# Performance work log

Measured on AMD Instinct MI355X. Metric: run time of the kernel, lower is better.

The kernel has to match this reference:

```python
import jax, jax.numpy as jnp
import numpy as np
from jax import lax

BN_EPS = 1e-5


def conv3x3(x, w):
    # x: [B,C,H,W], w: [O,I,3,3] -> [B,O,H,W], stride 1, SAME padding, no bias
    return lax.conv_general_dilated(x, w, (1, 1), 'SAME',
                                    dimension_numbers=('NCHW', 'OIHW', 'NCHW'))


def batchnorm_eval(x, gamma, beta, mean, var):
    inv = gamma / jnp.sqrt(var + BN_EPS)
    return x * inv[None, :, None, None] + (beta - mean * inv)[None, :, None, None]


def avg_pool3(x):
    # AvgPool2d(3, stride=1, padding=1) with count_include_pad=True -> sum/9
    s = lax.reduce_window(x, 0.0, lax.add, (1, 1, 3, 3), (1, 1, 1, 1), 'SAME')
    return s / 9.0


def max_pool3(x):
    return lax.reduce_window(x, -jnp.inf, lax.max, (1, 1, 3, 3), (1, 1, 1, 1), 'SAME')


def setup_inputs() -> dict:
    key = jax.random.key(0)
    ks = jax.random.split(key, 20)
    B, C, H, W = 8, 256, 48, 48
    sc = 0.05
    inp = {
        'ftr': jax.random.normal(ks[0], (B, C, H, W), jnp.float32),
        'wq': jax.random.normal(ks[1], (C, C, 1, 1), jnp.float32) * sc,
        'bq': jax.random.normal(ks[2], (C,), jnp.float32) * sc,
        'wk': jax.random.normal(ks[3], (C, C, 1, 1), jnp.float32) * sc,
        'bk': jax.random.normal(ks[4], (C,), jnp.float32) * sc,
        'wv': jax.random.normal(ks[5], (C, C, 1, 1), jnp.float32) * sc,
        'bv': jax.random.normal(ks[6], (C,), jnp.float32) * sc,
        'delta': jnp.array([0.1], jnp.float32),
        'w_rbc': jax.random.normal(ks[7], (C, C, 3, 3), jnp.float32) * sc,
        'g1': jnp.ones((C,), jnp.float32),
        'b1': jnp.zeros((C,), jnp.float32),
        'm1': jnp.zeros((C,), jnp.float32),
        'v1': jnp.ones((C,), jnp.float32),
        'w_rbc2': jax.random.normal(ks[8], (C, 2 * C, 3, 3), jnp.float32) * sc,
        'g2': jnp.ones((C,), jnp.float32),
        'b2': jnp.zeros((C,), jnp.float32),
        'm2': jnp.zeros((C,), jnp.float32),
        'v2': jnp.ones((C,), jnp.float32),
    }
    return inp


def reference(ftr, wq, bq, wk, bk, wv, bv, delta, w_rbc, g1, b1, m1, v1,
              w_rbc2, g2, b2, m2, v2):
    B, C, H, W = ftr.shape
    P = H * W
    x = ftr.reshape(B, C, P)  # [B,C,P]
    # 1x1 convs as channel matmuls
    q = jnp.einsum('oc,bcp->bop', wq[:, :, 0, 0], x) + bq[None, :, None]
    k = jnp.einsum('oc,bcp->bop', wk[:, :, 0, 0], x) + bk[None, :, None]
    v = jnp.einsum('oc,bcp->bop', wv[:, :, 0, 0], x) + bv[None, :, None]
    # scores[b,i,j] = sum_c q[b,c,i] * k[b,c,j]; softmax over i (dim=1)
    scores = jnp.einsum('bci,bcj->bij', q, k)
    weights = jax.nn.softmax(scores, axis=1)
    G = jnp.einsum('bci,bij->bcj', v, weights).reshape(B, C, H, W)
    out = delta[0] * G + ftr
    # conv_rbc: conv3x3 -> BN(eval) -> ReLU, then sigmoid gate
    out = jax.nn.relu(batchnorm_eval(conv3x3(out, w_rbc), g1, b1, m1, v1))
    gate = jax.nn.sigmoid(out)
    ftr_avg = avg_pool3(ftr) * gate
    ftr_max = max_pool3(ftr) * gate
    cat = jnp.concatenate((ftr_max, ftr_avg), axis=1)  # [B,2C,H,W]
    out = jax.nn.relu(batchnorm_eval(conv3x3(cat, w_rbc2), g2, b2, m2, v2))
    return out
```

## Files before the change

### kernel.cpp

```cpp
#include <hip/hip_runtime.h>
#include <math.h>

#define NB   8
#define CCH  256
#define PPX  2304
#define CPb  (CCH*PPX)
#define NTOT (NB*CPb)
#define PSQ  (PPX*PPX)
#define PADIMG 2500

typedef short short8_t __attribute__((ext_vector_type(8)));
typedef float f4_t __attribute__((ext_vector_type(4)));

__device__ __forceinline__ float relu_(float x){ return x > 0.f ? x : 0.f; }

__device__ __forceinline__ unsigned short f2bf(float f) {
  unsigned int u = __builtin_bit_cast(unsigned int, f);
  u += 0x7fffu + ((u >> 16) & 1u);
  return (unsigned short)(u >> 16);
}
__device__ __forceinline__ float bf2f(unsigned short h) {
  unsigned int u = ((unsigned int)h) << 16;
  return __builtin_bit_cast(float, u);
}
__device__ __forceinline__ unsigned int pack2(float a, float b) {
  return (unsigned int)f2bf(a) | ((unsigned int)f2bf(b) << 16);
}

__device__ __forceinline__ void gll16(const void* g, void* l) {
  __builtin_amdgcn_global_load_lds(
      (const __attribute__((address_space(1))) unsigned int*)g,
      (__attribute__((address_space(3))) unsigned int*)l, 16, 0, 0);
}

__global__ __launch_bounds__(256) void castw(
    const float* __restrict__ w, unsigned short* __restrict__ o, int n)
{
  const int i = blockIdx.x * 256 + threadIdx.x;
  if (i < n) o[i] = f2bf(w[i]);
}

__global__ __launch_bounds__(256) void repack_w(
    const float* __restrict__ w, unsigned short* __restrict__ wr, int Cin)
{
  const int idx = blockIdx.x * 256 + threadIdx.x;
  const int total = 9 * 256 * Cin;
  if (idx >= total) return;
  const int c = idx % Cin;
  const int rest = idx / Cin;
  const int o = rest % 256;
  const int tap = rest / 256;
  wr[idx] = f2bf(w[((size_t)o * Cin + c) * 9 + tap]);
}

__global__ __launch_bounds__(256) void transpose_cast(
    const float* __restrict__ ftr, unsigned short* __restrict__ xt)
{
  const int p0 = blockIdx.x * 64, c0 = blockIdx.y * 64, b = blockIdx.z;
  const int t = threadIdx.x;
  __shared__ unsigned short T[64][72];
  #pragma unroll
  for (int pass = 0; pass < 4; pass++) {
    const int cr = pass * 16 + (t >> 4);
    const int pc = (t & 15) * 4;
    float4 v = *(const float4*)&ftr[((size_t)(b * 256 + c0 + cr)) * PPX + p0 + pc];
    T[pc + 0][cr] = f2bf(v.x); T[pc + 1][cr] = f2bf(v.y);
    T[pc + 2][cr] = f2bf(v.z); T[pc + 3][cr] = f2bf(v.w);
  }
  __syncthreads();
  #pragma unroll
  for (int pass = 0; pass < 2; pass++) {
    const int pr = pass * 32 + (t >> 3);
    const int cc = (t & 7) * 8;
    *(uint4*)&xt[((size_t)(b * PPX + p0 + pr)) * 256 + c0 + cc] = *(const uint4*)&T[pr][cc];
  }
}

template<int EPI>
__global__ __launch_bounds__(256) void gemm_nt(
    const unsigned short* __restrict__ A, long Ab,
    const unsigned short* __restrict__ B, long Bb, int K,
    unsigned short* __restrict__ O, long Ob, int ldo,
    const float* __restrict__ bias,
    const float* __restrict__ ftr, const float* __restrict__ delta, int bstart)
{
  const int t = threadIdx.x;
  const int ln = t & 63;
  const int wid = t >> 6;
  const int wm = (wid & 1) * 64, wn = (wid >> 1) * 64;
  const int lm = ln & 15, lg = ln >> 4;
  const int m0 = blockIdx.x * 128, n0 = blockIdx.y * 128;
  const long bz = blockIdx.z;
  const unsigned short* Ap = A + bz * Ab;
  const unsigned short* Bp = B + bz * Bb;

  __shared__ __align__(16) unsigned short As[128 * 32];
  __shared__ __align__(16) unsigned short Bs[128 * 32];

  const int sR = ln >> 2, sP = ln & 3;
  const int fbase = lm * 32 + (((lg + (lm >> 2)) & 3) * 8);

  f4_t acc[4][4];
  #pragma unroll
  for (int i = 0; i < 4; i++)
    #pragma unroll
    for (int j = 0; j < 4; j++) acc[i][j] = (f4_t){0.f, 0.f, 0.f, 0.f};

  for (int k0 = 0; k0 < K; k0 += 32) {
    __syncthreads();
    #pragma unroll
    for (int i = wid; i < 8; i += 4) {
      const int R = i * 16 + sR;
      const int l = (sP - (R >> 2)) & 3;
      gll16(Ap + (size_t)(m0 + R) * K + k0 + l * 8, As + i * 512);
      gll16(Bp + (size_t)(n0 + R) * K + k0 + l * 8, Bs + i * 512);
    }
    __syncthreads();
    short8_t a[4], b[4];
    #pragma unroll
    for (int ti = 0; ti < 4; ti++)
      a[ti] = *(const short8_t*)(As + (wm + ti * 16) * 32 + fbase);
    #pragma unroll
    for (int tj = 0; tj < 4; tj++)
      b[tj] = *(const short8_t*)(Bs + (wn + tj * 16) * 32 + fbase);
    #pragma unroll
    for (int ti = 0; ti < 4; ti++)
      #pragma unroll
      for (int tj = 0; tj < 4; tj++)
        acc[ti][tj] = __builtin_amdgcn_mfma_f32_16x16x32_bf16(
            a[ti], b[tj], acc[ti][tj], 0, 0, 0);
  }

  if (EPI == 3) {
    const int b = bstart + (int)bz;
    const float d0 = delta[0];
    #pragma unroll
    for (int ti = 0; ti < 4; ti++) {
      const int mb = m0 + wm + ti * 16 + (lg << 2);
      #pragma unroll
      for (int tj = 0; tj < 4; tj++) {
        const int n = n0 + wn + tj * 16 + lm;
        const int y = n / 48, x = n - (n / 48) * 48;
        const size_t pp = (size_t)(y + 1) * 50 + (x + 1);
        float vr[4];
        #pragma unroll
        for (int r = 0; r < 4; r++)
          vr[r] = d0 * acc[ti][tj][r] + ftr[((size_t)(b * 256 + mb + r)) * PPX + n];
        uint2 o;
        o.x = pack2(vr[0], vr[1]);
        o.y = pack2(vr[2], vr[3]);
        *(uint2*)(O + ((size_t)b * PADIMG + pp) * 256 + mb) = o;
      }
    }
  } else {
    #pragma unroll
    for (int ti = 0; ti < 4; ti++) {
      const int mb = m0 + wm + ti * 16 + (lg << 2);
      #pragma unroll
      for (int tj = 0; tj < 4; tj++) {
        const int n = n0 + wn + tj * 16 + lm;
        float add0 = 0.f, add1 = 0.f, add2 = 0.f, add3 = 0.f;
        if (EPI == 1) { add0 = bias[mb]; add1 = bias[mb+1]; add2 = bias[mb+2]; add3 = bias[mb+3]; }
        if (EPI == 2) { add0 = add1 = add2 = add3 = bias[n]; }
        uint2 o;
        o.x = pack2(acc[ti][tj][0] + add0, acc[ti][tj][1] + add1);
        o.y = pack2(acc[ti][tj][2] + add2, acc[ti][tj][3] + add3);
        *(uint2*)(O + bz * Ob + (size_t)n * ldo + mb) = o;
      }
    }
  }
}

template<int EPI>
__global__ __launch_bounds__(256) void gemm64(
    const unsigned short* __restrict__ A, long Ab,
    const unsigned short* __restrict__ B, long Bb, int K,
    unsigned short* __restrict__ O, long Ob, int ldo,
    const float* __restrict__ bias,
    const float* __restrict__ ftr, const float* __restrict__ delta, int bstart)
{
  const int t = threadIdx.x;
  const int ln = t & 63;
  const int wid = t >> 6;
  const int wn = wid * 32;
  const int lm = ln & 15, lg = ln >> 4;
  const int m0 = blockIdx.x * 64, n0 = blockIdx.y * 128;
  const long bz = blockIdx.z;
  const unsigned short* Ap = A + bz * Ab;
  const unsigned short* Bp = B + bz * Bb;

  __shared__ __align__(16) unsigned short As[64 * 32];
  __shared__ __align__(16) unsigned short Bs[128 * 32];

  const int sR = ln >> 2, sP = ln & 3;
  const int fbase = lm * 32 + (((lg + (lm >> 2)) & 3) * 8);

  f4_t acc[4][2];
  #pragma unroll
  for (int i = 0; i < 4; i++)
    #pragma unroll
    for (int j = 0; j < 2; j++) acc[i][j] = (f4_t){0.f, 0.f, 0.f, 0.f};

  for (int k0 = 0; k0 < K; k0 += 32) {
    __syncthreads();
    {
      const int R = wid * 16 + sR;
      const int l = (sP - (R >> 2)) & 3;
      gll16(Ap + (size_t)(m0 + R) * K + k0 + l * 8, As + wid * 512);
    }
    #pragma unroll
    for (int i = wid; i < 8; i += 4) {
      const int R = i * 16 + sR;
      const int l = (sP - (R >> 2)) & 3;
      gll16(Bp + (size_t)(n0 + R) * K + k0 + l * 8, Bs + i * 512);
    }
    __syncthreads();
    short8_t a[4], b[2];
    #pragma unroll
    for (int ti = 0; ti < 4; ti++)
      a[ti] = *(const short8_t*)(As + (ti * 16) * 32 + fbase);
    #pragma unroll
    for (int tj = 0; tj < 2; tj++)
      b[tj] = *(const short8_t*)(Bs + (wn + tj * 16) * 32 + fbase);
    #pragma unroll
    for (int ti = 0; ti < 4; ti++)
      #pragma unroll
      for (int tj = 0; tj < 2; tj++)
        acc[ti][tj] = __builtin_amdgcn_mfma_f32_16x16x32_bf16(
            a[ti], b[tj], acc[ti][tj], 0, 0, 0);
  }

  if (EPI == 3) {
    const int b = bstart + (int)bz;
    const float d0 = delta[0];
    #pragma unroll
    for (int ti = 0; ti < 4; ti++) {
      const int mb = m0 + ti * 16 + (lg << 2);
      #pragma unroll
      for (int tj = 0; tj < 2; tj++) {
        const int n = n0 + wn + tj * 16 + lm;
        const int y = n / 48, x = n - (n / 48) * 48;
        const size_t pp = (size_t)(y + 1) * 50 + (x + 1);
        float vr[4];
        #pragma unroll
        for (int r = 0; r < 4; r++)
          vr[r] = d0 * acc[ti][tj][r] + ftr[((size_t)(b * 256 + mb + r)) * PPX + n];
        uint2 o;
        o.x = pack2(vr[0], vr[1]);
        o.y = pack2(vr[2], vr[3]);
        *(uint2*)(O + ((size_t)b * PADIMG + pp) * 256 + mb) = o;
      }
    }
  } else {
    #pragma unroll
    for (int ti = 0; ti < 4; ti++) {
      const int mb = m0 + ti * 16 + (lg << 2);
      #pragma unroll
      for (int tj = 0; tj < 2; tj++) {
        const int n = n0 + wn + tj * 16 + lm;
        float add0 = 0.f, add1 = 0.f, add2 = 0.f, add3 = 0.f;
        if (EPI == 1) { add0 = bias[mb]; add1 = bias[mb+1]; add2 = bias[mb+2]; add3 = bias[mb+3]; }
        if (EPI == 2) { add0 = add1 = add2 = add3 = bias[n]; }
        uint2 o;
        o.x = pack2(acc[ti][tj][0] + add0, acc[ti][tj][1] + add1);
        o.y = pack2(acc[ti][tj][2] + add2, acc[ti][tj][3] + add3);
        *(uint2*)(O + bz * Ob + (size_t)n * ldo + mb) = o;
      }
    }
  }
}

__global__ __launch_bounds__(256) void rowstats(
    unsigned short* __restrict__ St, long sstride)
{
  const int j = blockIdx.x, bb = blockIdx.y;
  unsigned short* row = St + (long)bb * sstride + (size_t)j * PPX;
  const int t = threadIdx.x;

  float v[16];
  int nv = 0;
  float m = -1e30f;
  for (int ch = t; ch < 288; ch += 256) {
    const uint4 d = *(const uint4*)(row + ch * 8);
    const unsigned int* dp = (const unsigned int*)&d;
    #pragma unroll
    for (int q = 0; q < 4; q++) {
      v[nv]     = bf2f((unsigned short)(dp[q] & 0xffffu));
      v[nv + 1] = bf2f((unsigned short)(dp[q] >> 16));
      m = fmaxf(m, fmaxf(v[nv], v[nv + 1]));
      nv += 2;
    }
  }
  #pragma unroll
  for (int off = 32; off > 0; off >>= 1)
    m = fmaxf(m, __shfl_xor(m, off));
  __shared__ float red[8];
  if ((t & 63) == 0) red[t >> 6] = m;
  __syncthreads();
  m = fmaxf(fmaxf(red[0], red[1]), fmaxf(red[2], red[3]));

  float sum = 0.f;
  for (int u = 0; u < nv; u++) { v[u] = __expf(v[u] - m); sum += v[u]; }
  #pragma unroll
  for (int off = 32; off > 0; off >>= 1)
    sum += __shfl_xor(sum, off);
  if ((t & 63) == 0) red[4 + (t >> 6)] = sum;
  __syncthreads();
  const float inv = 1.f / (red[4] + red[5] + red[6] + red[7]);

  int u = 0;
  for (int ch = t; ch < 288; ch += 256) {
    unsigned int res[4];
    #pragma unroll
    for (int q = 0; q < 4; q++) {
      res[q] = pack2(v[u] * inv, v[u + 1] * inv);
      u += 2;
    }
    *(uint4*)(row + ch * 8) = *(const uint4*)res;
  }
}

template<bool OUT_BF16>
__global__ __launch_bounds__(256) void conv_mfma(
    const unsigned short* __restrict__ act_p, int Cin,
    const unsigned short* __restrict__ wr,
    const float* __restrict__ gamma, const float* __restrict__ beta,
    const float* __restrict__ mean,  const float* __restrict__ var,
    void* __restrict__ outv)
{
  const int t  = threadIdx.x;
  const int wv = t >> 6;
  const int ln = t & 63;
  const int lm = ln & 15;
  const int lg = ln >> 4;

  const int bx = blockIdx.x;
  const int bb = bx / 9;
  const int p0 = (bx % 9) * 256;
  const int m0 = blockIdx.y * 32;

  __shared__ __align__(16) unsigned short As[9 * 32 * 32];
  __shared__ __align__(16) unsigned short Bs[368 * 32];

  const int qbase = p0 + 2 * (p0 / 48);
  int qoff[4];
  #pragma unroll
  for (int tj = 0; tj < 4; tj++) {
    const int p = p0 + wv * 64 + tj * 16 + lm;
    qoff[tj] = (p - p0) + 2 * (p / 48 - p0 / 48) + 51;
  }

  const int sR = ln >> 2, sP = ln & 3;
  const int sl = (sP - (sR >> 2)) & 3;
  const int abase = lm * 32 + (((lg + (lm >> 2)) & 3) * 8);

  const unsigned short* gb = act_p + (size_t)bb * PADIMG * Cin;
  const unsigned short* gsrc = gb + (size_t)(qbase + sR) * Cin + sl * 8;

  f4_t acc[2][4];
  #pragma unroll
  for (int i = 0; i < 2; i++)
    #pragma unroll
    for (int j = 0; j < 4; j++) acc[i][j] = (f4_t){0.f, 0.f, 0.f, 0.f};

  for (int c0 = 0; c0 < Cin; c0 += 32) {
    __syncthreads();
    for (int i = wv; i < 18; i += 4) {
      const int R = i * 16 + sR;
      const int tap = R >> 5, mr = R & 31;
      const int l = (sP - (R >> 2)) & 3;
      gll16(wr + ((size_t)(tap * 256 + m0 + mr)) * Cin + c0 + l * 8, As + i * 512);
    }
    const unsigned short* src = gsrc + c0;
    for (int i = wv; i < 23; i += 4)
      gll16(src + (size_t)i * 16 * Cin, Bs + i * 512);
    __syncthreads();
    #pragma unroll
    for (int ky = 0; ky < 3; ky++) {
      #pragma unroll
      for (int kx = 0; kx < 3; kx++) {
        const int off = (ky - 1) * 50 + (kx - 1);
        const int tap = ky * 3 + kx;
        short8_t a[2], b[4];
        #pragma unroll
        for (int ti = 0; ti < 2; ti++)
          a[ti] = *(const short8_t*)(As + tap * 1024 + ti * 512 + abase);
        #pragma unroll
        for (int tj = 0; tj < 4; tj++) {
          const int R = qoff[tj] + off;
          const int slot = (lg + (R >> 2)) & 3;
          b[tj] = *(const short8_t*)(Bs + R * 32 + slot * 8);
        }
        #pragma unroll
        for (int ti = 0; ti < 2; ti++)
          #pragma unroll
          for (int tj = 0; tj < 4; tj++)
            acc[ti][tj] = __builtin_amdgcn_mfma_f32_16x16x32_bf16(
                a[ti], b[tj], acc[ti][tj], 0, 0, 0);
      }
    }
  }

  #pragma unroll
  for (int ti = 0; ti < 2; ti++) {
    const int m = m0 + ti * 16 + (lg << 2);
    float inv[4], add[4];
    #pragma unroll
    for (int r = 0; r < 4; r++) {
      inv[r] = gamma[m + r] * rsqrtf(var[m + r] + 1e-5f);
      add[r] = beta[m + r] - mean[m + r] * inv[r];
    }
    #pragma unroll
    for (int tj = 0; tj < 4; tj++) {
      const int p = p0 + wv * 64 + tj * 16 + lm;
      float vr[4];
      #pragma unroll
      for (int r = 0; r < 4; r++)
        vr[r] = relu_(acc[ti][tj][r] * inv[r] + add[r]);
      if (OUT_BF16) {
        uint2 o;
        o.x = pack2(vr[0], vr[1]);
        o.y = pack2(vr[2], vr[3]);
        *(uint2*)((unsigned short*)outv + ((size_t)(bb * PPX + p)) * 256 + m) = o;
      } else {
        #pragma unroll
        for (int r = 0; r < 4; r++)
          ((float*)outv)[((size_t)(bb * 256 + m + r)) * PPX + p] = vr[r];
      }
    }
  }
}

__global__ __launch_bounds__(256) void pool_gate_cat(
    const unsigned short* __restrict__ xt, const unsigned short* __restrict__ act1b,
    unsigned short* __restrict__ cat_p)
{
  const int idx = blockIdx.x * 256 + threadIdx.x;
  const int c = idx & 255;
  const int rest = idx >> 8;
  const int p = rest % PPX;
  const int b = rest / PPX;
  const int y = p / 48, x = p - (p / 48) * 48;
  const unsigned short* base = xt + ((size_t)b * PPX) * 256 + c;
  float s = 0.f, mxv = -1e30f;
  #pragma unroll
  for (int dy = -1; dy <= 1; dy++) {
    const int yy = y + dy;
    if (yy < 0 || yy >= 48) continue;
    #pragma unroll
    for (int dx = -1; dx <= 1; dx++) {
      const int xx = x + dx;
      if (xx < 0 || xx >= 48) continue;
      const float f = bf2f(base[(size_t)(yy * 48 + xx) * 256]);
      s += f; mxv = fmaxf(mxv, f);
    }
  }
  const float g = bf2f(act1b[(size_t)idx]);
  const float gate = 1.f / (1.f + __expf(-g));
  const size_t pp = (size_t)(y + 1) * 50 + (x + 1);
  unsigned short* crow = cat_p + ((size_t)b * PADIMG + pp) * 512;
  crow[c]       = f2bf(mxv * gate);
  crow[c + 256] = f2bf(s * (1.f / 9.f) * gate);
}

extern "C" void kernel_launch(void* const* d_in, const int* in_sizes, int n_in,
                              void* d_out, int out_size, void* d_ws, size_t ws_size,
                              hipStream_t stream)
{
  const float* ftr  = (const float*)d_in[0];
  const float* wq   = (const float*)d_in[1];
  const float* bq   = (const float*)d_in[2];
  const float* wk   = (const float*)d_in[3];
  const float* bk   = (const float*)d_in[4];
  const float* wv   = (const float*)d_in[5];
  const float* bv   = (const float*)d_in[6];
  const float* delta= (const float*)d_in[7];
  const float* w1   = (const float*)d_in[8];
  const float* g1   = (const float*)d_in[9];
  const float* b1   = (const float*)d_in[10];
  const float* m1   = (const float*)d_in[11];
  const float* v1   = (const float*)d_in[12];
  const float* w2   = (const float*)d_in[13];
  const float* g2   = (const float*)d_in[14];
  const float* b2   = (const float*)d_in[15];
  const float* m2   = (const float*)d_in[16];
  const float* v2   = (const float*)d_in[17];
  float* out = (float*)d_out;

  const size_t XT = (size_t)NTOT;
  unsigned short* base = (unsigned short*)d_ws;
  unsigned short* xt   = base;
  unsigned short* qt   = xt  + XT;
  unsigned short* kt   = qt  + XT;
  unsigned short* vbuf = kt  + XT;
  unsigned short* wqb  = vbuf + XT;
  unsigned short* wkb  = wqb + 65536;
  unsigned short* wvb  = wkb + 65536;
  unsigned short* wr1  = wvb + 65536;
  unsigned short* wr2  = wr1 + (size_t)9 * 256 * 256;
  unsigned short* attn_p = wr2 + (size_t)9 * 256 * 512;
  unsigned short* act1b  = attn_p + (size_t)NB * PADIMG * 256;
  unsigned short* cat_p  = act1b + XT;
  unsigned short* St     = cat_p + (size_t)NB * PADIMG * 512;

  const size_t head_bytes = (size_t)((char*)St - (char*)base);
  const bool modeA = ws_size >= head_bytes + (size_t)NB * PSQ * 2;

  const size_t ATTN_P_SH = (size_t)NB * PADIMG * 256;
  const size_t CAT_P_SH  = (size_t)NB * PADIMG * 512;

  castw<<<dim3(256), 256, 0, stream>>>(wq, wqb, 65536);
  castw<<<dim3(256), 256, 0, stream>>>(wk, wkb, 65536);
  castw<<<dim3(256), 256, 0, stream>>>(wv, wvb, 65536);
  repack_w<<<dim3((9 * 256 * 256 + 255) / 256), 256, 0, stream>>>(w1, wr1, 256);
  repack_w<<<dim3((9 * 256 * 512 + 255) / 256), 256, 0, stream>>>(w2, wr2, 512);

  transpose_cast<<<dim3(36, 4, 8), 256, 0, stream>>>(ftr, xt);

  gemm64<1><<<dim3(4, 18, 8), 256, 0, stream>>>(
      wqb, 0L, xt, (long)CPb, 256, qt, (long)CPb, 256, bq, nullptr, nullptr, 0);
  gemm64<1><<<dim3(4, 18, 8), 256, 0, stream>>>(
      wkb, 0L, xt, (long)CPb, 256, kt, (long)CPb, 256, bk, nullptr, nullptr, 0);
  gemm64<2><<<dim3(36, 2, 8), 256, 0, stream>>>(
      xt, (long)CPb, wvb, 0L, 256, vbuf, (long)CPb, PPX, bv, nullptr, nullptr, 0);

  hipMemsetAsync(attn_p, 0, ATTN_P_SH * 2, stream);

  if (modeA) {
    gemm_nt<0><<<dim3(18, 18, 8), 256, 0, stream>>>(
        qt, (long)CPb, kt, (long)CPb, 256, St, (long)PSQ, PPX, nullptr, nullptr, nullptr, 0);
    rowstats<<<dim3(PPX, 8), 256, 0, stream>>>(St, (long)PSQ);
    gemm64<3><<<dim3(4, 18, 8), 256, 0, stream>>>(
        vbuf, (long)CPb, St, (long)PSQ, PPX, attn_p, 0L, 0, nullptr, ftr, delta, 0);
  } else {
    for (int b = 0; b < NB; b++) {
      gemm_nt<0><<<dim3(18, 18, 1), 256, 0, stream>>>(
          qt + (size_t)b * CPb, 0L, kt + (size_t)b * CPb, 0L, 256,
          St, 0L, PPX, nullptr, nullptr, nullptr, 0);
      rowstats<<<dim3(PPX, 1), 256, 0, stream>>>(St, 0L);
      gemm64<3><<<dim3(4, 18, 1), 256, 0, stream>>>(
          vbuf + (size_t)b * CPb, 0L, St, 0L, PPX, attn_p, 0L, 0, nullptr, ftr, delta, b);
    }
  }

  conv_mfma<true><<<dim3(72, 8), 256, 0, stream>>>(
      attn_p, 256, wr1, g1, b1, m1, v1, (void*)act1b);

  hipMemsetAsync(cat_p, 0, CAT_P_SH * 2, stream);
  pool_gate_cat<<<dim3(NTOT / 256), 256, 0, stream>>>(xt, act1b, cat_p);

  conv_mfma<false><<<dim3(72, 8), 256, 0, stream>>>(
      cat_p, 512, wr2, g2, b2, m2, v2, (void*)out);
}
```

Before: 434.4 us.

## Fuse softmax exp and normalization into PV GEMM, rowstats writes only max/sum

The rowstats kernel now writes only the per-row max and inverse sum, not the full normalized score matrix. A new 128x128-tile PV GEMM recomputes exp(s - max) on the fly while loading score tiles and applies the 1/sum scaling in the epilogue together with the delta-residual add. This drops one full read-modify-write pass over the large B×P×P score matrix. In exchange the GEMM does extra exp work per element, and each P tile is re-exponentiated for both channel blocks. The stats buffer reuses the wq weight buffer, which is no longer needed at that point.

```diff
diff --git a/kernel.cpp b/kernel.cpp
--- a/kernel.cpp
+++ b/kernel.cpp
@@ -131,28 +131,7 @@
             a[ti], b[tj], acc[ti][tj], 0, 0, 0);
   }
 
-  if (EPI == 3) {
-    const int b = bstart + (int)bz;
-    const float d0 = delta[0];
-    #pragma unroll
-    for (int ti = 0; ti < 4; ti++) {
-      const int mb = m0 + wm + ti * 16 + (lg << 2);
-      #pragma unroll
-      for (int tj = 0; tj < 4; tj++) {
-        const int n = n0 + wn + tj * 16 + lm;
-        const int y = n / 48, x = n - (n / 48) * 48;
-        const size_t pp = (size_t)(y + 1) * 50 + (x + 1);
-        float vr[4];
-        #pragma unroll
-        for (int r = 0; r < 4; r++)
-          vr[r] = d0 * acc[ti][tj][r] + ftr[((size_t)(b * 256 + mb + r)) * PPX + n];
-        uint2 o;
-        o.x = pack2(vr[0], vr[1]);
-        o.y = pack2(vr[2], vr[3]);
-        *(uint2*)(O + ((size_t)b * PADIMG + pp) * 256 + mb) = o;
-      }
-    }
-  } else {
+  {
     #pragma unroll
     for (int ti = 0; ti < 4; ti++) {
       const int mb = m0 + wm + ti * 16 + (lg << 2);
@@ -171,6 +150,100 @@
   }
 }
 
+__global__ __launch_bounds__(256) void gemm_pv(
+    const unsigned short* __restrict__ A, long Ab,
+    const unsigned short* __restrict__ B, long Bb,
+    int K,
+    unsigned short* __restrict__ O,
+    const float* __restrict__ stats,
+    const float* __restrict__ ftr, const float* __restrict__ delta, int bstart)
+{
+  const int t = threadIdx.x;
+  const int ln = t & 63;
+  const int wid = t >> 6;
+  const int wm = (wid & 1) * 64, wn = (wid >> 1) * 64;
+  const int lm = ln & 15, lg = ln >> 4;
+  const int m0 = blockIdx.x * 128, n0 = blockIdx.y * 128;
+  const long bz = blockIdx.z;
+  const int b = bstart + (int)bz;
+  const unsigned short* Ap = A + bz * Ab;
+  const unsigned short* Bp = B + bz * Bb;
+
+  __shared__ __align__(16) unsigned short As[128 * 32];
+  __shared__ __align__(16) unsigned short Bs[128 * 32];
+
+  const int sR = ln >> 2, sP = ln & 3;
+  const int fbase = lm * 32 + (((lg + (lm >> 2)) & 3) * 8);
+
+  float mj[4], ivj[4];
+  #pragma unroll
+  for (int tj = 0; tj < 4; tj++) {
+    const int n = n0 + wn + tj * 16 + lm;
+    const float2 s2 = *(const float2*)&stats[((size_t)b * PPX + n) * 2];
+    mj[tj] = s2.x; ivj[tj] = s2.y;
+  }
+
+  f4_t acc[4][4];
+  #pragma unroll
+  for (int i = 0; i < 4; i++)
+    #pragma unroll
+    for (int j = 0; j < 4; j++) acc[i][j] = (f4_t){0.f, 0.f, 0.f, 0.f};
+
+  for (int k0 = 0; k0 < K; k0 += 32) {
+    __syncthreads();
+    #pragma unroll
+    for (int i = wid; i < 8; i += 4) {
+      const int R = i * 16 + sR;
+      const int l = (sP - (R >> 2)) & 3;
+      gll16(Ap + (size_t)(m0 + R) * K + k0 + l * 8, As + i * 512);
+      gll16(Bp + (size_t)(n0 + R) * K + k0 + l * 8, Bs + i * 512);
+    }
+    __syncthreads();
+    short8_t a[4], b8[4];
+    #pragma unroll
+    for (int ti = 0; ti < 4; ti++)
+      a[ti] = *(const short8_t*)(As + (wm + ti * 16) * 32 + fbase);
+    #pragma unroll
+    for (int tj = 0; tj < 4; tj++) {
+      short8_t raw = *(const short8_t*)(Bs + (wn + tj * 16) * 32 + fbase);
+      short8_t w;
+      #pragma unroll
+      for (int e = 0; e < 8; e++) {
+        const float f = bf2f((unsigned short)raw[e]);
+        w[e] = (short)f2bf(__expf(f - mj[tj]));
+      }
+      b8[tj] = w;
+    }
+    #pragma unroll
+    for (int ti = 0; ti < 4; ti++)
+      #pragma unroll
+      for (int tj = 0; tj < 4; tj++)
+        acc[ti][tj] = __builtin_amdgcn_mfma_f32_16x16x32_bf16(
+            a[ti], b8[tj], acc[ti][tj], 0, 0, 0);
+  }
+
+  const float d0 = delta[0];
+  #pragma unroll
+  for (int ti = 0; ti < 4; ti++) {
+    const int mb = m0 + wm + ti * 16 + (lg << 2);
+    #pragma unroll
+    for (int tj = 0; tj < 4; tj++) {
+      const int n = n0 + wn + tj * 16 + lm;
+      const int y = n / 48, x = n - (n / 48) * 48;
+      const size_t pp = (size_t)(y + 1) * 50 + (x + 1);
+      const float sc = d0 * ivj[tj];
+      float vr[4];
+      #pragma unroll
+      for (int r = 0; r < 4; r++)
+        vr[r] = sc * acc[ti][tj][r] + ftr[((size_t)(b * 256 + mb + r)) * PPX + n];
+      uint2 o;
+      o.x = pack2(vr[0], vr[1]);
+      o.y = pack2(vr[2], vr[3]);
+      *(uint2*)(O + ((size_t)b * PADIMG + pp) * 256 + mb) = o;
+    }
+  }
+}
+
 template<int EPI>
 __global__ __launch_bounds__(256) void gemm64(
     const unsigned short* __restrict__ A, long Ab,
@@ -230,28 +303,7 @@
             a[ti], b[tj], acc[ti][tj], 0, 0, 0);
   }
 
-  if (EPI == 3) {
-    const int b = bstart + (int)bz;
-    const float d0 = delta[0];
-    #pragma unroll
-    for (int ti = 0; ti < 4; ti++) {
-      const int mb = m0 + ti * 16 + (lg << 2);
-      #pragma unroll
-      for (int tj = 0; tj < 2; tj++) {
-        const int n = n0 + wn + tj * 16 + lm;
-        const int y = n / 48, x = n - (n / 48) * 48;
-        const size_t pp = (size_t)(y + 1) * 50 + (x + 1);
-        float vr[4];
-        #pragma unroll
-        for (int r = 0; r < 4; r++)
-          vr[r] = d0 * acc[ti][tj][r] + ftr[((size_t)(b * 256 + mb + r)) * PPX + n];
-        uint2 o;
-        o.x = pack2(vr[0], vr[1]);
-        o.y = pack2(vr[2], vr[3]);
-        *(uint2*)(O + ((size_t)b * PADIMG + pp) * 256 + mb) = o;
-      }
-    }
-  } else {
+  {
     #pragma unroll
     for (int ti = 0; ti < 4; ti++) {
       const int mb = m0 + ti * 16 + (lg << 2);
@@ -271,10 +323,11 @@
 }
 
 __global__ __launch_bounds__(256) void rowstats(
-    unsigned short* __restrict__ St, long sstride)
+    const unsigned short* __restrict__ St, long sstride,
+    float* __restrict__ stats, int bstart)
 {
   const int j = blockIdx.x, bb = blockIdx.y;
-  unsigned short* row = St + (long)bb * sstride + (size_t)j * PPX;
+  const unsigned short* row = St + (long)bb * sstride + (size_t)j * PPX;
   const int t = threadIdx.x;
 
   float v[16];
@@ -300,23 +353,16 @@
   m = fmaxf(fmaxf(red[0], red[1]), fmaxf(red[2], red[3]));
 
   float sum = 0.f;
-  for (int u = 0; u < nv; u++) { v[u] = __expf(v[u] - m); sum += v[u]; }
+  for (int u = 0; u < nv; u++) sum += __expf(v[u] - m);
   #pragma unroll
   for (int off = 32; off > 0; off >>= 1)
     sum += __shfl_xor(sum, off);
   if ((t & 63) == 0) red[4 + (t >> 6)] = sum;
   __syncthreads();
-  const float inv = 1.f / (red[4] + red[5] + red[6] + red[7]);
-
-  int u = 0;
-  for (int ch = t; ch < 288; ch += 256) {
-    unsigned int res[4];
-    #pragma unroll
-    for (int q = 0; q < 4; q++) {
-      res[q] = pack2(v[u] * inv, v[u + 1] * inv);
-      u += 2;
-    }
-    *(uint4*)(row + ch * 8) = *(const uint4*)res;
+  if (t == 0) {
+    const float tot = red[4] + red[5] + red[6] + red[7];
+    float2 out; out.x = m; out.y = 1.f / tot;
+    *(float2*)&stats[((size_t)(bstart + bb) * PPX + j) * 2] = out;
   }
 }
 
@@ -503,6 +549,8 @@
   unsigned short* cat_p  = act1b + XT;
   unsigned short* St     = cat_p + (size_t)NB * PADIMG * 512;
 
+  float* stats = (float*)wqb;
+
   const size_t head_bytes = (size_t)((char*)St - (char*)base);
   const bool modeA = ws_size >= head_bytes + (size_t)NB * PSQ * 2;
 
@@ -529,17 +577,17 @@
   if (modeA) {
     gemm_nt<0><<<dim3(18, 18, 8), 256, 0, stream>>>(
         qt, (long)CPb, kt, (long)CPb, 256, St, (long)PSQ, PPX, nullptr, nullptr, nullptr, 0);
-    rowstats<<<dim3(PPX, 8), 256, 0, stream>>>(St, (long)PSQ);
-    gemm64<3><<<dim3(4, 18, 8), 256, 0, stream>>>(
-        vbuf, (long)CPb, St, (long)PSQ, PPX, attn_p, 0L, 0, nullptr, ftr, delta, 0);
+    rowstats<<<dim3(PPX, 8), 256, 0, stream>>>(St, (long)PSQ, stats, 0);
+    gemm_pv<<<dim3(2, 18, 8), 256, 0, stream>>>(
+        vbuf, (long)CPb, St, (long)PSQ, PPX, attn_p, stats, ftr, delta, 0);
   } else {
     for (int b = 0; b < NB; b++) {
       gemm_nt<0><<<dim3(18, 18, 1), 256, 0, stream>>>(
           qt + (size_t)b * CPb, 0L, kt + (size_t)b * CPb, 0L, 256,
           St, 0L, PPX, nullptr, nullptr, nullptr, 0);
-      rowstats<<<dim3(PPX, 1), 256, 0, stream>>>(St, 0L);
-      gemm64<3><<<dim3(4, 18, 1), 256, 0, stream>>>(
-          vbuf + (size_t)b * CPb, 0L, St, 0L, PPX, attn_p, 0L, 0, nullptr, ftr, delta, b);
+      rowstats<<<dim3(PPX, 1), 256, 0, stream>>>(St, 0L, stats, b);
+      gemm_pv<<<dim3(2, 18, 1), 256, 0, stream>>>(
+          vbuf + (size_t)b * CPb, 0L, St, 0L, PPX, attn_p, stats, ftr, delta, b);
     }
   }
 
```

Measured after the change: 460.6 us. 1.06x slower.
